# Performance work log

Measured on AMD Instinct MI355X. Metric: run time of the kernel, lower is better.

## Reference

```python
import jax, jax.numpy as jnp
import numpy as np

N = 4096
INP_DIM = 256
EMB_DIM = 256
ALPHA = 0.01  # LeakyReLU negative slope
NEG_INF = -9.0e15


def _xavier(key, shape, gain=1.414):
    fan_in, fan_out = shape[0], shape[1]
    limit = gain * np.sqrt(6.0 / (fan_in + fan_out))
    return jax.random.uniform(key, shape, jnp.float32, -limit, limit)


def setup_inputs() -> dict:
    key = jax.random.key(0)
    ks = jax.random.split(key, 9)
    inp = {
        "input": jax.random.normal(ks[0], (N, INP_DIM), jnp.float32),
        "adj": jax.random.randint(ks[1], (N, N), 0, 2, jnp.int32),
        "W0": _xavier(ks[2], (INP_DIM, EMB_DIM)),
        "W1": _xavier(ks[3], (EMB_DIM, EMB_DIM)),
        "a1": _xavier(ks[4], (2 * EMB_DIM, 1)),
        "W2": _xavier(ks[5], (EMB_DIM, EMB_DIM)),
        "a2": _xavier(ks[6], (2 * EMB_DIM, 1)),
        "W3": _xavier(ks[7], (EMB_DIM, EMB_DIM)),
        "a3": _xavier(ks[8], (2 * EMB_DIM, 1)),
    }
    return inp


def _gat_layer(h, adj, W, a):
    # h: [N, F_in], W: [F_in, F], a: [2F, 1]
    Wh = h @ W                       # [N, F]
    F_out = Wh.shape[1]
    # e_ij = leakyrelu([Wh_i || Wh_j] @ a) = leakyrelu(Wh_i@a1 + Wh_j@a2)
    f1 = Wh @ a[:F_out]              # [N, 1]
    f2 = Wh @ a[F_out:]              # [N, 1]
    e = jax.nn.leaky_relu(f1 + f2.T, ALPHA)            # [N, N]
    att = jnp.where(adj > 0, e, NEG_INF)
    att = jax.nn.softmax(att, axis=1)                    # masked softmax over neighbors
    h_prime = att @ Wh                                   # [N, F]
    return jax.nn.elu(h_prime)                           # concat=True -> ELU


def reference(input, adj, W0, W1, a1, W2, a2, W3, a3):
    h = input @ W0                   # GAT-level projection
    h = _gat_layer(h, adj, W1, a1)
    h = _gat_layer(h, adj, W2, a2)
    h = _gat_layer(h, adj, W3, a3)
    return h
```

## Files before the change

### kernel.cpp

```cpp
#include <hip/hip_runtime.h>
#include <hip/hip_bf16.h>
#include <hip/hip_fp16.h>
#include <cstdint>
#include <cstddef>

#define NN 4096
#define FD 256
#define WPR 64

typedef __attribute__((ext_vector_type(8))) unsigned short ushort8v;
typedef __attribute__((ext_vector_type(4))) unsigned short ushort4v;
typedef __attribute__((ext_vector_type(8))) short short8;
typedef __attribute__((ext_vector_type(4))) float float4v;

#define C1 30.0f
#define C2 0.3f

static __device__ __forceinline__ unsigned short f2bf(float x) {
    union { float f; unsigned int u; } v; v.f = x;
    unsigned int r = v.u + 0x7FFFu + ((v.u >> 16) & 1u);
    return (unsigned short)(r >> 16);
}

static __device__ __forceinline__ short8 as_s8(ushort8v v) {
    union { ushort8v u; short8 s; } x; x.u = v; return x.s;
}

__global__ __launch_bounds__(256) void setup(const int* __restrict__ adj,
                                             const float* __restrict__ input,
                                             const float* __restrict__ W0, const float* __restrict__ W1,
                                             const float* __restrict__ W2, const float* __restrict__ W3,
                                             unsigned long long* __restrict__ bits,
                                             unsigned short* __restrict__ hb,
                                             unsigned short* __restrict__ Wbt,
                                             float* __restrict__ f1f2) {
    const int b = blockIdx.x;
    const int t = threadIdx.x;
    if (b < 4096) {
        const int wave = t >> 6, lane = t & 63;
        const int* arow = adj + (size_t)b * NN;
        #pragma unroll
        for (int it = 0; it < NN / 256; ++it) {
            int j = it * 256 + wave * 64 + lane;
            unsigned long long m = __ballot(arow[j] > 0);
            if (lane == 0) bits[(size_t)b * WPR + (it * 4 + wave)] = m;
        }
        hb[(size_t)b * 256 + t] = f2bf(input[(size_t)b * 256 + t]);
    } else if (b < 5120) {
        int idx = (b - 4096) * 256 + t;
        int mat = idx >> 16;
        int within = idx & 65535;
        int n = within >> 8, k = within & 255;
        const float* W = (mat == 0) ? W0 : (mat == 1) ? W1 : (mat == 2) ? W2 : W3;
        Wbt[idx] = f2bf(W[k * 256 + n]);
    } else {
        #pragma unroll
        for (int i = 0; i < 24; ++i) {
            int pos = i * 1024 + (b - 5120) * 256 + t;
            f1f2[pos] = 0.f;
        }
    }
}

__global__ __launch_bounds__(256) void proj_gemm(const unsigned short* __restrict__ A,
                                                 const unsigned short* __restrict__ Bt,
                                                 const float* __restrict__ av,
                                                 float* __restrict__ f1f2,
                                                 unsigned short* __restrict__ Cbt,
                                                 unsigned short* __restrict__ Crow) {
    const int t = threadIdx.x;
    const int bm = blockIdx.x >> 2, bn = blockIdx.x & 3;
    const int m0 = bm * 32, n0 = bn * 64;
    __shared__ unsigned short As[32 * 264];
    __shared__ unsigned short Bs[64 * 264];
    const int lane = t & 63, wave = t >> 6;
    const int wm = (wave >> 1) * 16, wn = (wave & 1) * 32;
    const int g = lane >> 4, ml = lane & 15;
    {
        int ar = t >> 3, ac0 = (t & 7) * 8;
        #pragma unroll
        for (int i = 0; i < 4; ++i) {
            int col = ac0 + i * 64;
            *(ushort8v*)&As[ar * 264 + col] = *(const ushort8v*)&A[(size_t)(m0 + ar) * 256 + col];
        }
        int br = t >> 2, bc0 = (t & 3) * 8;
        #pragma unroll
        for (int i = 0; i < 8; ++i) {
            int col = bc0 + i * 32;
            *(ushort8v*)&Bs[br * 264 + col] = *(const ushort8v*)&Bt[(size_t)(n0 + br) * 256 + col];
        }
    }
    __syncthreads();
    float4v acc[2] = {{0.f,0.f,0.f,0.f},{0.f,0.f,0.f,0.f}};
    #pragma unroll
    for (int kk = 0; kk < 256; kk += 32) {
        const int kc = kk + g * 8;
        short8 a = as_s8(*(const ushort8v*)&As[(wm + ml) * 264 + kc]);
        #pragma unroll
        for (int fn = 0; fn < 2; ++fn) {
            short8 b = as_s8(*(const ushort8v*)&Bs[(wn + fn * 16 + ml) * 264 + kc]);
            acc[fn] = __builtin_amdgcn_mfma_f32_16x16x32_bf16(a, b, acc[fn], 0, 0, 0);
        }
    }

    const int rb = wm + g * 4;
    if (Crow) {
        #pragma unroll
        for (int fn = 0; fn < 2; ++fn)
            #pragma unroll
            for (int r = 0; r < 4; ++r)
                Crow[(size_t)(m0 + rb + r) * 256 + n0 + wn + fn * 16 + ml] = f2bf(acc[fn][r]);
    }

    if (f1f2) {
        float a1c[2], a2c[2];
        #pragma unroll
        for (int fn = 0; fn < 2; ++fn) {
            a1c[fn] = av[n0 + wn + fn * 16 + ml];
            a2c[fn] = av[256 + n0 + wn + fn * 16 + ml];
        }
        #pragma unroll
        for (int r = 0; r < 4; ++r) {
            float s1 = acc[0][r] * a1c[0] + acc[1][r] * a1c[1];
            float s2 = acc[0][r] * a2c[0] + acc[1][r] * a2c[1];
            #pragma unroll
            for (int off = 1; off < 16; off <<= 1) {
                s1 += __shfl_xor(s1, off, 64);
                s2 += __shfl_xor(s2, off, 64);
            }
            if (ml == 0) {
                int row = m0 + rb + r;
                atomicAdd(&f1f2[row], s1);
                atomicAdd(&f1f2[4096 + row], s2);
            }
        }
    }

    if (Cbt) {
        unsigned short* T = As;
        __syncthreads();
        #pragma unroll
        for (int fn = 0; fn < 2; ++fn)
            #pragma unroll
            for (int r = 0; r < 4; ++r)
                T[(wn + fn * 16 + ml) * 40 + rb + r] = f2bf(acc[fn][r]);
        __syncthreads();
        const int tr = t >> 2, tc = (t & 3) * 8;
        *(ushort8v*)&Cbt[(size_t)(n0 + tr) * 4096 + m0 + tc] = *(const ushort8v*)&T[tr * 40 + tc];
    }
}

__global__ __launch_bounds__(256) void rowcoef(const unsigned long long* __restrict__ bits,
                                               const float* __restrict__ f1f2,
                                               float4* __restrict__ rowco,
                                               float2* __restrict__ tab2g) {
    __shared__ float2 tl[4096];
    const int t = threadIdx.x;
    const float* f2p = f1f2 + 4096;
    #pragma unroll
    for (int i = 0; i < 16; ++i) {
        float v = f2p[i * 256 + t];
        float2 pr = make_float2(__expf(v - C1), __expf(0.01f * v - C2));
        tl[i * 256 + t] = pr;
        if (blockIdx.x == 0) tab2g[i * 256 + t] = pr;
    }
    __syncthreads();
    const int lane = t & 63, wave = t >> 6;
    for (int rr = 0; rr < 2; ++rr) {
        const int row = blockIdx.x * 8 + wave * 2 + rr;
        const unsigned long long wl = bits[(size_t)row * WPR + lane];
        const float f1r = f1f2[row];
        const float th = __expf(-f1r - C1);
        float mx = 0.f, S1 = 0.f, S2 = 0.f;
        #pragma unroll 16
        for (int b = 0; b < 64; ++b) {
            unsigned long long w = __shfl(wl, b, 64);
            bool bit = (w >> lane) & 1ULL;
            float2 v = tl[b * 64 + lane];
            float ebm = bit ? v.x : 0.f;
            mx = fmaxf(mx, ebm);
            bool cond = v.x > th;
            S1 += (bit && cond)  ? v.x : 0.f;
            S2 += (bit && !cond) ? v.y : 0.f;
        }
        #pragma unroll
        for (int off = 1; off < 64; off <<= 1) {
            mx = fmaxf(mx, __shfl_xor(mx, off, 64));
            S1 += __shfl_xor(S1, off, 64);
            S2 += __shfl_xor(S2, off, 64);
        }
        if (lane == 0) {
            float M  = C1 + __logf(mx);
            float fm_ = f1r + M;
            float m  = fm_ > 0.f ? fm_ : 0.01f * fm_;
            float alpha = __expf(fminf(f1r + C1 - m, 60.f));
            float gamma = __expf(fminf(0.01f * (f1r + C1) - m, 60.f));
            float inv = 1.0f / (alpha * S1 + gamma * S2);
            rowco[row] = make_float4(alpha * inv, gamma * inv, th, 0.f);
        }
    }
}

template<int NSTEPS>
__global__ __launch_bounds__(256, 3) void att_gemm(const unsigned long long* __restrict__ bits,
                                                   const float4* __restrict__ rowco,
                                                   const float* __restrict__ tab2f,
                                                   const unsigned short* __restrict__ Bt,
                                                   unsigned short* __restrict__ parth) {
    const int t = threadIdx.x;
    const int bm = blockIdx.x & 31;
    const int bn = (blockIdx.x >> 5) & 1;
    const int ks = blockIdx.x >> 6;
    const int m0 = bm * 128, n0 = bn * 128;
    const int k0 = ks * (NSTEPS * 32);
    __shared__ unsigned short Bs[2][128 * 40];
    const int lane = t & 63, wave = t >> 6;
    const int g = lane >> 4, ml = lane & 15;
    const int srow = t >> 1, skh = (t & 1) * 16;
    const unsigned short* bsrc = Bt + (size_t)(n0 + srow) * 4096 + skh;

    float pA[2], pG[2];
    unsigned long long wpre[2][NSTEPS / 2];
    #pragma unroll
    for (int fm = 0; fm < 2; ++fm) {
        int row = m0 + wave * 32 + fm * 16 + ml;
        float4 rc = rowco[row];
        pA[fm] = rc.x; pG[fm] = rc.y;
        const unsigned long long* brow = bits + (size_t)row * WPR + (k0 >> 6);
        #pragma unroll
        for (int w = 0; w < NSTEPS / 2; ++w) wpre[fm][w] = brow[w];
    }

    float4v acc[2][8];
    #pragma unroll
    for (int i = 0; i < 2; ++i)
        #pragma unroll
        for (int j = 0; j < 8; ++j) acc[i][j] = (float4v){0.f, 0.f, 0.f, 0.f};

    float4v tq0, tq1, tq2, tq3;
    {
        ushort8v b0 = *(const ushort8v*)&bsrc[k0];
        ushort8v b1 = *(const ushort8v*)&bsrc[k0 + 8];
        const float4v* q = (const float4v*)&tab2f[2 * (k0 + g * 8)];
        tq0 = q[0]; tq1 = q[1]; tq2 = q[2]; tq3 = q[3];
        *(ushort8v*)&Bs[0][srow * 40 + skh]     = b0;
        *(ushort8v*)&Bs[0][srow * 40 + skh + 8] = b1;
    }
    __syncthreads();

    #pragma unroll
    for (int i = 0; i < NSTEPS; ++i) {
        const int kk = k0 + i * 32;
        const int p = i & 1;
        ushort8v nb0, nb1;
        float4v nt0, nt1, nt2, nt3;
        if (i + 1 < NSTEPS) {
            nb0 = *(const ushort8v*)&bsrc[kk + 32];
            nb1 = *(const ushort8v*)&bsrc[kk + 40];
            const float4v* q = (const float4v*)&tab2f[2 * (kk + 32 + g * 8)];
            nt0 = q[0]; nt1 = q[1]; nt2 = q[2]; nt3 = q[3];
        }
        const int sh = (i & 1) * 32 + g * 8;
        short8 afr[2];
        #pragma unroll
        for (int fm = 0; fm < 2; ++fm) {
            unsigned int wh = (unsigned int)(wpre[fm][i >> 1] >> sh);
            ushort8v af;
            #pragma unroll
            for (int jj = 0; jj < 4; ++jj) {
                float4v v = (jj == 0) ? tq0 : (jj == 1) ? tq1 : (jj == 2) ? tq2 : tq3;
                float x0 = fmaxf(pA[fm] * v[0], pG[fm] * v[1]);
                float x1 = fmaxf(pA[fm] * v[2], pG[fm] * v[3]);
                x0 = ((wh >> (2 * jj)) & 1u)     ? x0 : 0.f;
                x1 = ((wh >> (2 * jj + 1)) & 1u) ? x1 : 0.f;
                union { __hip_bfloat162 b2; unsigned int u; } cv;
                cv.b2 = __float22bfloat162_rn(make_float2(x0, x1));
                ((unsigned int*)&af)[jj] = cv.u;
            }
            afr[fm] = as_s8(af);
        }
        #pragma unroll
        for (int fn = 0; fn < 8; ++fn) {
            short8 b = as_s8(*(const ushort8v*)&Bs[p][(fn * 16 + ml) * 40 + g * 8]);
            acc[0][fn] = __builtin_amdgcn_mfma_f32_16x16x32_bf16(afr[0], b, acc[0][fn], 0, 0, 0);
            acc[1][fn] = __builtin_amdgcn_mfma_f32_16x16x32_bf16(afr[1], b, acc[1][fn], 0, 0, 0);
        }
        if (i + 1 < NSTEPS) {
            *(ushort8v*)&Bs[1 - p][srow * 40 + skh]     = nb0;
            *(ushort8v*)&Bs[1 - p][srow * 40 + skh + 8] = nb1;
            __syncthreads();
            tq0 = nt0; tq1 = nt1; tq2 = nt2; tq3 = nt3;
        }
    }

    unsigned short* pbase = parth + ((size_t)ks << 20) + (size_t)(bm * 2 + bn) * 16384;
    #pragma unroll
    for (int fm = 0; fm < 2; ++fm)
        #pragma unroll
        for (int fn = 0; fn < 8; ++fn) {
            ushort4v v4;
            #pragma unroll
            for (int r = 0; r < 4; ++r) {
                __half h = __float2half(acc[fm][fn][r]);
                v4[r] = *(unsigned short*)&h;
            }
            *(ushort4v*)&pbase[((wave * 16 + fm * 8 + fn) * 64 + lane) * 4] = v4;
        }
}

template<int NS>
__global__ __launch_bounds__(256) void att_reduce(const unsigned short* __restrict__ parth,
                                                  float* __restrict__ outf,
                                                  unsigned short* __restrict__ hrow) {
    const int flat = (blockIdx.x * 256 + threadIdx.x) * 8;
    float s[8] = {0.f, 0.f, 0.f, 0.f, 0.f, 0.f, 0.f, 0.f};
    #pragma unroll
    for (int sp = 0; sp < NS; ++sp) {
        ushort8v v = *(const ushort8v*)&parth[((size_t)sp << 20) + flat];
        #pragma unroll
        for (int j = 0; j < 8; ++j) {
            unsigned short u = v[j];
            s[j] += __half2float(*(__half*)&u);
        }
    }
    const int tile  = flat >> 14;
    const int inner = flat & 16383;
    const int widx = inner >> 8;
    const int ls   = (inner >> 2) & 63;
    const int bm = tile >> 1, bn = tile & 1;
    const int wavea = widx >> 4, fm = (widx >> 3) & 1, fn = widx & 7;
    const int g = ls >> 4, ml = ls & 15;
    const int row0 = bm * 128 + wavea * 32 + fm * 16 + g * 4;
    const int col  = bn * 128 + fn * 16 + ml;
    #pragma unroll
    for (int r = 0; r < 4; ++r) {
        float x0 = s[r];
        float x1 = s[4 + r];
        x0 = x0 > 0.f ? x0 : (__expf(x0) - 1.f);
        x1 = x1 > 0.f ? x1 : (__expf(x1) - 1.f);
        unsigned int hp = (unsigned int)f2bf(x0) | ((unsigned int)f2bf(x1) << 16);
        *(unsigned int*)&hrow[(size_t)(row0 + r) * 256 + col] = hp;
        if (outf) *(float2*)&outf[(size_t)(row0 + r) * 256 + col] = make_float2(x0, x1);
    }
}

static void launch_att(int SPLIT, const unsigned long long* bits, const float4* rowco,
                       const float* tab2f, const unsigned short* Bt,
                       unsigned short* parth, hipStream_t stream) {
    if (SPLIT == 16) att_gemm<8><<<64 * 16, 256, 0, stream>>>(bits, rowco, tab2f, Bt, parth);
    else             att_gemm<16><<<64 * 8, 256, 0, stream>>>(bits, rowco, tab2f, Bt, parth);
}

static void launch_reduce(int SPLIT, const unsigned short* parth, float* outf,
                          unsigned short* hrow, hipStream_t stream) {
    if (SPLIT == 16) att_reduce<16><<<512, 256, 0, stream>>>(parth, outf, hrow);
    else             att_reduce<8><<<512, 256, 0, stream>>>(parth, outf, hrow);
}

extern "C" void kernel_launch(void* const* d_in, const int* in_sizes, int n_in,
                              void* d_out, int out_size, void* d_ws, size_t ws_size,
                              hipStream_t stream) {
    const float* input = (const float*)d_in[0];
    const int*   adj   = (const int*)d_in[1];
    const float* W0    = (const float*)d_in[2];
    const float* W1    = (const float*)d_in[3];
    const float* a1    = (const float*)d_in[4];
    const float* W2    = (const float*)d_in[5];
    const float* a2    = (const float*)d_in[6];
    const float* W3    = (const float*)d_in[7];
    const float* a3    = (const float*)d_in[8];
    float* out = (float*)d_out;
    char* ws = (char*)d_ws;

    unsigned long long* bits = (unsigned long long*)(ws);
    unsigned short* h0   = (unsigned short*)(ws + (2u << 20));
    unsigned short* h1   = (unsigned short*)(ws + (4u << 20));
    unsigned short* Whbt = (unsigned short*)(ws + (6u << 20));
    unsigned short* Wbt  = (unsigned short*)(ws + (8u << 20));
    float*  f1f2  = (float*)(ws + (9u << 20));
    float4* rowco = (float4*)(ws + (10u << 20));
    float2* tab2  = (float2*)(ws + (10u << 20) + (256u << 10));
    unsigned short* parth = (unsigned short*)(ws + (13u << 20));

    const size_t base = 13u << 20;
    int SPLIT = (base + 16u * (2u << 20) <= ws_size) ? 16 : 8;

    float* f1f2_l[3] = { f1f2, f1f2 + 8192, f1f2 + 16384 };

    setup<<<5124, 256, 0, stream>>>(adj, input, W0, W1, W2, W3, bits, h0, Wbt, f1f2);

    proj_gemm<<<512, 256, 0, stream>>>(h0, Wbt + 0 * 65536, nullptr, nullptr, nullptr, h1);

    proj_gemm<<<512, 256, 0, stream>>>(h1, Wbt + 1 * 65536, a1, f1f2_l[0], Whbt, nullptr);
    rowcoef<<<512, 256, 0, stream>>>(bits, f1f2_l[0], rowco, tab2);
    launch_att(SPLIT, bits, rowco, (const float*)tab2, Whbt, parth, stream);
    launch_reduce(SPLIT, parth, nullptr, h0, stream);

    proj_gemm<<<512, 256, 0, stream>>>(h0, Wbt + 2 * 65536, a2, f1f2_l[1], Whbt, nullptr);
    rowcoef<<<512, 256, 0, stream>>>(bits, f1f2_l[1], rowco, tab2);
    launch_att(SPLIT, bits, rowco, (const float*)tab2, Whbt, parth, stream);
    launch_reduce(SPLIT, parth, nullptr, h1, stream);

    proj_gemm<<<512, 256, 0, stream>>>(h1, Wbt + 3 * 65536, a3, f1f2_l[2], Whbt, nullptr);
    rowcoef<<<512, 256, 0, stream>>>(bits, f1f2_l[2], rowco, tab2);
    launch_att(SPLIT, bits, rowco, (const float*)tab2, Whbt, parth, stream);
    launch_reduce(SPLIT, parth, out, h0, stream);
}
```

Baseline: 277.0 us.

## Fuse split-K reduction and ELU with next layer projection GEMM

Merges the partial-sum reduction, ELU and bf16 conversion of each attention layer into the following layer's projection GEMM. Each block reduces 16 rows into shared memory, multiplies by W with MFMA, accumulates the f1/f2 attention logits with atomics and writes the transposed Wh. This removes one kernel launch per layer and the round trip of the hidden state through global memory. In exchange it launches only 256 blocks, rereads B from global for every block, and relies on f1f2 being zeroed beforehand because the logits are now accumulated with atomics.

Result: no change. 277.3 us (+0.1%).

```diff
diff --git a/kernel.cpp b/kernel.cpp
--- a/kernel.cpp
+++ b/kernel.cpp
@@ -309,9 +309,112 @@
 }
 
 template<int NS>
-__global__ __launch_bounds__(256) void att_reduce(const unsigned short* __restrict__ parth,
-                                                  float* __restrict__ outf,
-                                                  unsigned short* __restrict__ hrow) {
+__global__ __launch_bounds__(256) void fused_rp(const unsigned short* __restrict__ parth,
+                                                const unsigned short* __restrict__ Bt,
+                                                const float* __restrict__ av,
+                                                float* __restrict__ f1f2,
+                                                unsigned short* __restrict__ Cbt) {
+    const int t = threadIdx.x;
+    const int m0 = blockIdx.x * 16;
+    __shared__ unsigned short hA[16 * 280];
+    __shared__ unsigned short T[256 * 24];
+
+    const int bmP = m0 >> 7;
+    const int wavea = (m0 >> 5) & 3;
+    const int fmP = (m0 >> 4) & 1;
+    const int bn = t >> 7, fnc = (t >> 4) & 7;
+    const int widx = wavea * 16 + fmP * 8 + fnc;
+    const size_t cbase = (size_t)(bmP * 2 + bn) * 16384 + (size_t)widx * 256 + (t & 15) * 16;
+    float s[16];
+    #pragma unroll
+    for (int e = 0; e < 16; ++e) s[e] = 0.f;
+    #pragma unroll
+    for (int sp = 0; sp < NS; ++sp) {
+        const unsigned short* p = &parth[((size_t)sp << 20) + cbase];
+        ushort8v v0 = *(const ushort8v*)p;
+        ushort8v v1 = *(const ushort8v*)(p + 8);
+        #pragma unroll
+        for (int e = 0; e < 8; ++e) {
+            unsigned short u0 = v0[e], u1 = v1[e];
+            s[e]     += __half2float(*(__half*)&u0);
+            s[8 + e] += __half2float(*(__half*)&u1);
+        }
+    }
+    const int gq = (t & 15) >> 2;
+    const int colb = bn * 128 + fnc * 16 + (t & 3) * 4;
+    #pragma unroll
+    for (int r = 0; r < 4; ++r) {
+        ushort4v w4;
+        #pragma unroll
+        for (int c = 0; c < 4; ++c) {
+            float x = s[c * 4 + r];
+            x = x > 0.f ? x : (__expf(x) - 1.f);
+            w4[c] = f2bf(x);
+        }
+        *(ushort4v*)&hA[(gq * 4 + r) * 280 + colb] = w4;
+    }
+    __syncthreads();
+
+    const int lane = t & 63, wave = t >> 6;
+    const int g = lane >> 4, ml = lane & 15;
+    float4v acc[4] = {{0.f,0.f,0.f,0.f},{0.f,0.f,0.f,0.f},{0.f,0.f,0.f,0.f},{0.f,0.f,0.f,0.f}};
+    #pragma unroll
+    for (int kk = 0; kk < 256; kk += 32) {
+        short8 a = as_s8(*(const ushort8v*)&hA[ml * 280 + kk + g * 8]);
+        #pragma unroll
+        for (int fn = 0; fn < 4; ++fn) {
+            short8 b = as_s8(*(const ushort8v*)&Bt[(size_t)(wave * 64 + fn * 16 + ml) * 256 + kk + g * 8]);
+            acc[fn] = __builtin_amdgcn_mfma_f32_16x16x32_bf16(a, b, acc[fn], 0, 0, 0);
+        }
+    }
+
+    {
+        float a1c[4], a2c[4];
+        #pragma unroll
+        for (int fn = 0; fn < 4; ++fn) {
+            int col = wave * 64 + fn * 16 + ml;
+            a1c[fn] = av[col];
+            a2c[fn] = av[256 + col];
+        }
+        #pragma unroll
+        for (int r = 0; r < 4; ++r) {
+            float s1 = acc[0][r] * a1c[0] + acc[1][r] * a1c[1] + acc[2][r] * a1c[2] + acc[3][r] * a1c[3];
+            float s2 = acc[0][r] * a2c[0] + acc[1][r] * a2c[1] + acc[2][r] * a2c[2] + acc[3][r] * a2c[3];
+            #pragma unroll
+            for (int off = 1; off < 16; off <<= 1) {
+                s1 += __shfl_xor(s1, off, 64);
+                s2 += __shfl_xor(s2, off, 64);
+            }
+            if (ml == 0) {
+                int row = m0 + g * 4 + r;
+                atomicAdd(&f1f2[row], s1);
+                atomicAdd(&f1f2[4096 + row], s2);
+            }
+        }
+    }
+
+    #pragma unroll
+    for (int fn = 0; fn < 4; ++fn) {
+        int nl = wave * 64 + fn * 16 + ml;
+        ushort4v v4;
+        #pragma unroll
+        for (int r = 0; r < 4; ++r) v4[r] = f2bf(acc[fn][r]);
+        *(ushort4v*)&T[nl * 24 + g * 4] = v4;
+    }
+    __syncthreads();
+    {
+        const int tn = t >> 1, half = t & 1;
+        #pragma unroll
+        for (int pass = 0; pass < 2; ++pass) {
+            int n = pass * 128 + tn;
+            *(ushort8v*)&Cbt[(size_t)n * 4096 + m0 + half * 8] = *(const ushort8v*)&T[n * 24 + half * 8];
+        }
+    }
+}
+
+template<int NS>
+__global__ __launch_bounds__(256) void reduce_out(const unsigned short* __restrict__ parth,
+                                                  float* __restrict__ outf) {
     const int flat = (blockIdx.x * 256 + threadIdx.x) * 8;
     float s[8] = {0.f, 0.f, 0.f, 0.f, 0.f, 0.f, 0.f, 0.f};
     #pragma unroll
@@ -338,9 +441,7 @@
         float x1 = s[4 + r];
         x0 = x0 > 0.f ? x0 : (__expf(x0) - 1.f);
         x1 = x1 > 0.f ? x1 : (__expf(x1) - 1.f);
-        unsigned int hp = (unsigned int)f2bf(x0) | ((unsigned int)f2bf(x1) << 16);
-        *(unsigned int*)&hrow[(size_t)(row0 + r) * 256 + col] = hp;
-        if (outf) *(float2*)&outf[(size_t)(row0 + r) * 256 + col] = make_float2(x0, x1);
+        *(float2*)&outf[(size_t)(row0 + r) * 256 + col] = make_float2(x0, x1);
     }
 }
 
@@ -351,10 +452,15 @@
     else             att_gemm<16><<<64 * 8, 256, 0, stream>>>(bits, rowco, tab2f, Bt, parth);
 }
 
-static void launch_reduce(int SPLIT, const unsigned short* parth, float* outf,
-                          unsigned short* hrow, hipStream_t stream) {
-    if (SPLIT == 16) att_reduce<16><<<512, 256, 0, stream>>>(parth, outf, hrow);
-    else             att_reduce<8><<<512, 256, 0, stream>>>(parth, outf, hrow);
+static void launch_frp(int SPLIT, const unsigned short* parth, const unsigned short* Bt,
+                       const float* av, float* f1f2, unsigned short* Cbt, hipStream_t stream) {
+    if (SPLIT == 16) fused_rp<16><<<256, 256, 0, stream>>>(parth, Bt, av, f1f2, Cbt);
+    else             fused_rp<8><<<256, 256, 0, stream>>>(parth, Bt, av, f1f2, Cbt);
+}
+
+static void launch_rout(int SPLIT, const unsigned short* parth, float* outf, hipStream_t stream) {
+    if (SPLIT == 16) reduce_out<16><<<512, 256, 0, stream>>>(parth, outf);
+    else             reduce_out<8><<<512, 256, 0, stream>>>(parth, outf);
 }
 
 extern "C" void kernel_launch(void* const* d_in, const int* in_sizes, int n_in,
@@ -394,15 +500,13 @@
     proj_gemm<<<512, 256, 0, stream>>>(h1, Wbt + 1 * 65536, a1, f1f2_l[0], Whbt, nullptr);
     rowcoef<<<512, 256, 0, stream>>>(bits, f1f2_l[0], rowco, tab2);
     launch_att(SPLIT, bits, rowco, (const float*)tab2, Whbt, parth, stream);
-    launch_reduce(SPLIT, parth, nullptr, h0, stream);
-
-    proj_gemm<<<512, 256, 0, stream>>>(h0, Wbt + 2 * 65536, a2, f1f2_l[1], Whbt, nullptr);
+
+    launch_frp(SPLIT, parth, Wbt + 2 * 65536, a2, f1f2_l[1], Whbt, stream);
     rowcoef<<<512, 256, 0, stream>>>(bits, f1f2_l[1], rowco, tab2);
     launch_att(SPLIT, bits, rowco, (const float*)tab2, Whbt, parth, stream);
-    launch_reduce(SPLIT, parth, nullptr, h1, stream);
-
-    proj_gemm<<<512, 256, 0, stream>>>(h1, Wbt + 3 * 65536, a3, f1f2_l[2], Whbt, nullptr);
+
+    launch_frp(SPLIT, parth, Wbt + 3 * 65536, a3, f1f2_l[2], Whbt, stream);
     rowcoef<<<512, 256, 0, stream>>>(bits, f1f2_l[2], rowco, tab2);
     launch_att(SPLIT, bits, rowco, (const float*)tab2, Whbt, parth, stream);
-    launch_reduce(SPLIT, parth, out, h0, stream);
-}
+    launch_rout(SPLIT, parth, out, stream);
+}
```
